# Kernel optimization log

Hardware: AMD Instinct MI355X
Metric: run time of the kernel (lower is better)

## Reference

```python
import jax, jax.numpy as jnp
import numpy as np

B, T, C = 2, 512, 128
H = 4 * C
EPS_LN = 1e-5
EPS_WKV = 1e-6


def setup_inputs() -> dict:
    key = jax.random.key(0)
    ks = jax.random.split(key, 12)
    def rn(i, shape, s):
        return jax.random.normal(ks[i], shape, jnp.float32) * s
    return {
        "x": jax.random.normal(ks[0], (B, T, C), jnp.float32),
        "ln1_g": jnp.ones((C,), jnp.float32), "ln1_b": jnp.zeros((C,), jnp.float32),
        "mu": rn(1, (C,), 0.1),
        "Wr": rn(2, (C, C), 0.02), "br": jnp.zeros((C,), jnp.float32),
        "Wk": rn(3, (C, C), 0.02), "bk": jnp.zeros((C,), jnp.float32),
        "Wv": rn(4, (C, C), 0.02), "bv": jnp.zeros((C,), jnp.float32),
        "w_decay": rn(5, (C,), 0.5),
        "Wo": rn(6, (C, C), 0.02), "bo": jnp.zeros((C,), jnp.float32),
        "ln2_g": jnp.ones((C,), jnp.float32), "ln2_b": jnp.zeros((C,), jnp.float32),
        "W1": rn(7, (C, H), 0.02), "b1": jnp.zeros((H,), jnp.float32),
        "W2": rn(8, (H, C), 0.02), "b2": jnp.zeros((C,), jnp.float32),
    }


def _ln(x, g, b):
    m = x.mean(-1, keepdims=True)
    v = ((x - m) ** 2).mean(-1, keepdims=True)
    return (x - m) * jax.lax.rsqrt(v + EPS_LN) * g + b


def _wkv_dir(k, v, w_lc):
    # k, v: (B,T,C); w_lc: (T,C) per-(position,channel) decay weight
    p = k[:, :, None, :] * w_lc[None, None, :, :]              # (B,T,L,C)
    p = jnp.exp(p - jax.lax.stop_gradient(p.max(-1, keepdims=True)))  # stable, max over C (as in source, dim=-1)
    p = p / (p.sum(-1, keepdims=True) + EPS_WKV)               # normalize over channel dim, as written in torch
    return jnp.einsum('btlc,blc->btc', p, v)


def _forward(x, ln1_g, ln1_b, mu, Wr, br, Wk, bk, Wv, bv, w_decay, Wo, bo, ln2_g, ln2_b, W1, b1, W2, b2):
    Tn = x.shape[1]
    h = _ln(x, ln1_g, ln1_b)
    # TemporalShift: past half shifted right, future half shifted left
    xp, xf = jnp.split(h, 2, axis=-1)
    xp = jnp.pad(xp, ((0, 0), (1, 0), (0, 0)))[:, :-1]
    xf = jnp.pad(xf, ((0, 0), (0, 1), (0, 0)))[:, 1:]
    hs = h + mu * jnp.concatenate([xp, xf], axis=-1)
    r = jax.nn.sigmoid(hs @ Wr + br)
    k = hs @ Wk + bk
    v = hs @ Wv + bv
    t = jnp.arange(Tn, dtype=x.dtype)[:, None]                 # (T,1)
    neg_w = -jnp.exp(w_decay)[None, :]                         # (1,C)
    w_f = neg_w * (Tn - 1 - t) / (Tn - 1)                      # (T,C)
    w_b = neg_w * t / (Tn - 1)                                 # (T,C)
    x_f = _wkv_dir(k, v, w_f)
    x_b = jnp.flip(_wkv_dir(jnp.flip(k, 1), jnp.flip(v, 1), w_b), 1)
    wk = r * (x_f + x_b) * 0.5
    y = x + wk @ Wo + bo
    h2 = _ln(y, ln2_g, ln2_b)
    m = jax.nn.gelu(h2 @ W1 + b1, approximate=False) @ W2 + b2
    return y + m


def reference(x, ln1_g, ln1_b, mu, Wr, br, Wk, bk, Wv, bv, w_decay, Wo, bo, ln2_g, ln2_b, W1, b1, W2, b2):
    return _forward(x, ln1_g, ln1_b, mu, Wr, br, Wk, bk, Wv, bv, w_decay, Wo, bo, ln2_g, ln2_b, W1, b1, W2, b2)
```

## Files before the change

kernel.cpp:

```cpp
#include <hip/hip_runtime.h>
#include <hip/hip_bf16.h>

#define Bq 2
#define Tq 512
#define Cq 128
#define Hq 512
#define NROW (Bq*Tq)

__device__ __forceinline__ float bfbits2f(unsigned short u) {
    return __uint_as_float(((unsigned)u) << 16);
}
__device__ __forceinline__ bool detect_f32(const void* sent) {
    return *(const unsigned*)sent == 0x3F800000u;
}
#define LD(p, i) (f32 ? ((const float*)(p))[i] : bfbits2f(((const unsigned short*)(p))[i]))
__device__ __forceinline__ float4 LD4(const void* p, int i, bool f32) {
    if (f32) return ((const float4*)p)[i >> 2];
    ushort4 u = *(const ushort4*)((const unsigned short*)p + i);
    return make_float4(bfbits2f(u.x), bfbits2f(u.y), bfbits2f(u.z), bfbits2f(u.w));
}

__global__ __launch_bounds__(512) void k2_qkv(
    const void* __restrict__ sent,
    const void* __restrict__ x,
    const void* __restrict__ ln1g, const void* __restrict__ ln1b,
    const void* __restrict__ mu,
    const void* __restrict__ Wr, const void* __restrict__ br,
    const void* __restrict__ Wk, const void* __restrict__ bk,
    const void* __restrict__ Wv, const void* __restrict__ bv,
    const void* __restrict__ wdec,
    float* __restrict__ r_out, float* __restrict__ u_out,
    float* __restrict__ v_out)
{
    const bool f32 = detect_f32(sent);
    int R0 = blockIdx.x * 2, tid = threadIdx.x;
    int g = tid >> 7, col = tid & 127;
    int t0 = R0 & (Tq - 1);
    int bbase = R0 - t0;

    __shared__ float h4[4][Cq];
    __shared__ float hs2[2][Cq];
    __shared__ float part[4][6][Cq];
    __shared__ float wred[8][2];

    {
        int t = t0 - 1 + g;
        int tcl = min(max(t, 0), Tq - 1);
        int row = bbase + tcl;
        float xv = LD(x, row * Cq + col);
        float s1 = xv, s2 = xv * xv;
        for (int off = 32; off; off >>= 1) {
            s1 += __shfl_xor(s1, off);
            s2 += __shfl_xor(s2, off);
        }
        int wid = tid >> 6;
        if ((tid & 63) == 0) { wred[wid][0] = s1; wred[wid][1] = s2; }
        __syncthreads();
        float S1 = wred[2 * g][0] + wred[2 * g + 1][0];
        float S2 = wred[2 * g][1] + wred[2 * g + 1][1];
        float m  = S1 * (1.f / Cq);
        float va = S2 * (1.f / Cq) - m * m;
        float rs = rsqrtf(va + 1e-5f);
        h4[g][col] = (xv - m) * rs * LD(ln1g, col) + LD(ln1b, col);
    }
    __syncthreads();

    if (g < 2) {
        int r2 = g, tt = t0 + r2;
        float hv = h4[r2 + 1][col];
        float nb;
        if (col < Cq / 2) nb = (tt > 0)      ? h4[r2][col]     : 0.f;
        else              nb = (tt < Tq - 1) ? h4[r2 + 2][col] : 0.f;
        hs2[r2][col] = hv + LD(mu, col) * nb;
    }
    __syncthreads();

    {
        float ar0 = 0.f, ar1 = 0.f, ak0 = 0.f, ak1 = 0.f, av0 = 0.f, av1 = 0.f;
        int c0 = g * 32;
        for (int cc = c0; cc < c0 + 32; cc += 4) {
            float4 h0 = *(const float4*)&hs2[0][cc];
            float4 h1 = *(const float4*)&hs2[1][cc];
            float wr0 = LD(Wr, (cc + 0) * Cq + col);
            float wr1 = LD(Wr, (cc + 1) * Cq + col);
            float wr2 = LD(Wr, (cc + 2) * Cq + col);
            float wr3 = LD(Wr, (cc + 3) * Cq + col);
            float wk0 = LD(Wk, (cc + 0) * Cq + col);
            float wk1 = LD(Wk, (cc + 1) * Cq + col);
            float wk2 = LD(Wk, (cc + 2) * Cq + col);
            float wk3 = LD(Wk, (cc + 3) * Cq + col);
            float wv0 = LD(Wv, (cc + 0) * Cq + col);
            float wv1 = LD(Wv, (cc + 1) * Cq + col);
            float wv2 = LD(Wv, (cc + 2) * Cq + col);
            float wv3 = LD(Wv, (cc + 3) * Cq + col);
            ar0 += h0.x * wr0; ar1 += h1.x * wr0;
            ak0 += h0.x * wk0; ak1 += h1.x * wk0;
            av0 += h0.x * wv0; av1 += h1.x * wv0;
            ar0 += h0.y * wr1; ar1 += h1.y * wr1;
            ak0 += h0.y * wk1; ak1 += h1.y * wk1;
            av0 += h0.y * wv1; av1 += h1.y * wv1;
            ar0 += h0.z * wr2; ar1 += h1.z * wr2;
            ak0 += h0.z * wk2; ak1 += h1.z * wk2;
            av0 += h0.z * wv2; av1 += h1.z * wv2;
            ar0 += h0.w * wr3; ar1 += h1.w * wr3;
            ak0 += h0.w * wk3; ak1 += h1.w * wk3;
            av0 += h0.w * wv3; av1 += h1.w * wv3;
        }
        part[g][0][col] = ar0; part[g][1][col] = ar1;
        part[g][2][col] = ak0; part[g][3][col] = ak1;
        part[g][4][col] = av0; part[g][5][col] = av1;
    }
    __syncthreads();

    if (g < 3) {
#pragma unroll
        for (int r2 = 0; r2 < 2; ++r2) {
            int m = 2 * g + r2;
            float a = (part[0][m][col] + part[1][m][col])
                    + (part[2][m][col] + part[3][m][col]);
            int row = R0 + r2;
            if (g == 0) {
                float rr = 1.f / (1.f + __expf(-(a + LD(br, col))));
                r_out[row * Cq + col] = rr;
            } else if (g == 1) {
                float wd = LD(wdec, col);
                wd = fminf(fmaxf(wd, -20.f), 20.f);
                float negw = -__expf(wd);
                float uu = (a + LD(bk, col)) * negw;
                uu = fminf(fmaxf(uu, -30.f), 30.f);
                u_out[row * Cq + col] = uu;
            } else {
                v_out[row * Cq + col] = a + LD(bv, col);
            }
        }
    }
}

__global__ __launch_bounds__(1024) void k34_wkv_ffn(
    const void* __restrict__ sent,
    const float* __restrict__ u_in,
    const float* __restrict__ v_in,
    const float* __restrict__ r_in,
    const void* __restrict__ x,
    const void* __restrict__ Wo, const void* __restrict__ bo,
    const void* __restrict__ lng, const void* __restrict__ lnb,
    const void* __restrict__ W1, const void* __restrict__ b1,
    const void* __restrict__ W2, const void* __restrict__ b2,
    void* __restrict__ out)
{
    const bool f32 = detect_f32(sent);
    int R0 = blockIdx.x * 4, tid = threadIdx.x;
    int b = R0 >> 9;
    const float inv511 = 1.f / (float)(Tq - 1);

    __shared__ float u4[4][Cq];
    __shared__ float rinv[4][Tq];
    __shared__ float vbuf[2][32][Cq];
    __shared__ float pp2[2][4][Cq];
    __shared__ float wk4[4][Cq];
    __shared__ float pwo[2][4][Cq];
    __shared__ float y4[4][Cq];
    __shared__ float h2s[4][Cq];
    __shared__ float part1[4][4][Hq];
    __shared__ float m1s[4][Hq];
    __shared__ float part2[8][4][Cq];
    __shared__ float wred[16][2];

    if (tid < 512) {
        int r = tid >> 7, c = tid & 127;
        u4[r][c] = u_in[(R0 + r) * Cq + c];
    }
    __syncthreads();

    {
        int l = tid & 511, rb = (tid >> 9) * 2;
        float a = (float)(Tq - 1 - l) * inv511 * 1.44269504f;
#pragma unroll
        for (int rr = rb; rr < rb + 2; ++rr) {
            float s0 = 0.f, s1 = 0.f, s2 = 0.f, s3 = 0.f;
            const float4* uu4 = (const float4*)u4[rr];
            for (int cc = 0; cc < Cq / 4; ++cc) {
                float4 uv = uu4[cc];
                s0 += exp2f(a * uv.x);
                s1 += exp2f(a * uv.y);
                s2 += exp2f(a * uv.z);
                s3 += exp2f(a * uv.w);
            }
            rinv[rr][l] = 1.f / ((s0 + s1) + (s2 + s3) + 1e-6f);
        }
    }

    const float4* v4g = (const float4*)v_in + (size_t)b * (Tq * Cq / 4);
    ((float4*)vbuf[0])[tid] = v4g[tid];
    __syncthreads();

    {
        int r = tid >> 8, h = (tid >> 7) & 1, c = tid & 127;
        float uu = u4[r][c];
        float gi1 = __expf(-uu * inv511);
        float gi2 = gi1 * gi1, gi3 = gi2 * gi1, gi4 = gi2 * gi2;
        float gi16 = gi4 * gi4; gi16 *= gi16;
        float gi32 = gi16 * gi16;
        float el0 = __expf(uu * (float)(Tq - 1 - 16 * h) * inv511);
        float a0 = 0.f, a1 = 0.f, a2 = 0.f, a3 = 0.f;
        for (int ci = 0; ci < 16; ++ci) {
            int cur = ci & 1;
            float4 vnext;
            if (ci < 15) vnext = v4g[(ci + 1) * 1024 + tid];
            int lb = ci * 32 + h * 16;
            int lloc = h * 16;
            float el = el0;
#pragma unroll
            for (int q = 0; q < 4; ++q) {
                float4 rv = *(const float4*)&rinv[r][lb + 4 * q];
                float v0 = vbuf[cur][lloc + 4 * q + 0][c];
                float v1 = vbuf[cur][lloc + 4 * q + 1][c];
                float v2 = vbuf[cur][lloc + 4 * q + 2][c];
                float v3 = vbuf[cur][lloc + 4 * q + 3][c];
                a0 += v0 * (el * rv.x);
                a1 += v1 * ((el * gi1) * rv.y);
                a2 += v2 * ((el * gi2) * rv.z);
                a3 += v3 * ((el * gi3) * rv.w);
                el *= gi4;
            }
            el0 *= gi32;
            if (ci < 15) ((float4*)vbuf[cur ^ 1])[tid] = vnext;
            __syncthreads();
        }
        pp2[h][r][c] = (a0 + a1) + (a2 + a3);
    }
    __syncthreads();

    if (tid < 512) {
        int r = tid >> 7, c = tid & 127;
        float acc = pp2[0][r][c] + pp2[1][r][c];
        wk4[r][c] = r_in[(R0 + r) * Cq + c] * acc;
    }
    __syncthreads();

    {
        int r = tid >> 8, ks = (tid >> 7) & 1, c = tid & 127;
        float s = 0.f;
        int k0 = ks * 64;
        for (int kk = k0; kk < k0 + 64; kk += 4) {
            float4 w = *(const float4*)&wk4[r][kk];
            s += w.x * LD(Wo, (kk + 0) * Cq + c);
            s += w.y * LD(Wo, (kk + 1) * Cq + c);
            s += w.z * LD(Wo, (kk + 2) * Cq + c);
            s += w.w * LD(Wo, (kk + 3) * Cq + c);
        }
        pwo[ks][r][c] = s;
    }
    __syncthreads();
    if (tid < 512) {
        int r = tid >> 7, c = tid & 127;
        y4[r][c] = LD(x, (R0 + r) * Cq + c) + pwo[0][r][c] + pwo[1][r][c] + LD(bo, c);
    }
    __syncthreads();

    {
        int r = tid >> 7, c = tid & 127;
        float yv = (tid < 512) ? y4[r][c] : 0.f;
        float s1 = yv, s2 = yv * yv;
        for (int off = 32; off; off >>= 1) {
            s1 += __shfl_xor(s1, off);
            s2 += __shfl_xor(s2, off);
        }
        int wid = tid >> 6;
        if ((tid & 63) == 0) { wred[wid][0] = s1; wred[wid][1] = s2; }
        __syncthreads();
        if (tid < 512) {
            float S1 = wred[2 * r][0] + wred[2 * r + 1][0];
            float S2 = wred[2 * r][1] + wred[2 * r + 1][1];
            float m  = S1 * (1.f / Cq);
            float va = S2 * (1.f / Cq) - m * m;
            float rs = rsqrtf(va + 1e-5f);
            h2s[r][c] = (yv - m) * rs * LD(lng, c) + LD(lnb, c);
        }
    }
    __syncthreads();

    {
        int ks = (tid >> 7) & 3, rh = tid >> 9, j4 = (tid & 127) * 4;
        int ra = 2 * rh, rb2 = 2 * rh + 1;
        float a00 = 0.f, a01 = 0.f, a02 = 0.f, a03 = 0.f;
        float a10 = 0.f, a11 = 0.f, a12 = 0.f, a13 = 0.f;
        int c0 = ks * 32;
        for (int cc = c0; cc < c0 + 32; cc += 4) {
            float4 w0 = LD4(W1, (cc + 0) * Hq + j4, f32);
            float4 w1 = LD4(W1, (cc + 1) * Hq + j4, f32);
            float4 w2 = LD4(W1, (cc + 2) * Hq + j4, f32);
            float4 w3 = LD4(W1, (cc + 3) * Hq + j4, f32);
            float4 ha = *(const float4*)&h2s[ra][cc];
            float4 hb = *(const float4*)&h2s[rb2][cc];
            a00 += ha.x * w0.x; a01 += ha.x * w0.y; a02 += ha.x * w0.z; a03 += ha.x * w0.w;
            a10 += hb.x * w0.x; a11 += hb.x * w0.y; a12 += hb.x * w0.z; a13 += hb.x * w0.w;
            a00 += ha.y * w1.x; a01 += ha.y * w1.y; a02 += ha.y * w1.z; a03 += ha.y * w1.w;
            a10 += hb.y * w1.x; a11 += hb.y * w1.y; a12 += hb.y * w1.z; a13 += hb.y * w1.w;
            a00 += ha.z * w2.x; a01 += ha.z * w2.y; a02 += ha.z * w2.z; a03 += ha.z * w2.w;
            a10 += hb.z * w2.x; a11 += hb.z * w2.y; a12 += hb.z * w2.z; a13 += hb.z * w2.w;
            a00 += ha.w * w3.x; a01 += ha.w * w3.y; a02 += ha.w * w3.z; a03 += ha.w * w3.w;
            a10 += hb.w * w3.x; a11 += hb.w * w3.y; a12 += hb.w * w3.z; a13 += hb.w * w3.w;
        }
        *(float4*)&part1[ks][ra][j4]  = make_float4(a00, a01, a02, a03);
        *(float4*)&part1[ks][rb2][j4] = make_float4(a10, a11, a12, a13);
    }
    __syncthreads();
    {
        int j = tid & 511, rh = tid >> 9;
        float bb = LD(b1, j);
#pragma unroll
        for (int rr = 2 * rh; rr < 2 * rh + 2; ++rr) {
            float xg = ((part1[0][rr][j] + part1[1][rr][j])
                      + (part1[2][rr][j] + part1[3][rr][j])) + bb;
            m1s[rr][j] = 0.5f * xg * (1.f + erff(xg * 0.70710678f));
        }
    }
    __syncthreads();

    {
        int ks = tid >> 7, c = tid & 127;
        int h0 = ks * 64;
        float a0 = 0.f, a1 = 0.f, a2 = 0.f, a3 = 0.f;
        for (int hh = h0; hh < h0 + 64; hh += 4) {
            float4 m0 = *(const float4*)&m1s[0][hh];
            float4 m1v = *(const float4*)&m1s[1][hh];
            float4 m2 = *(const float4*)&m1s[2][hh];
            float4 m3 = *(const float4*)&m1s[3][hh];
            float w0 = LD(W2, (hh + 0) * Cq + c);
            float w1 = LD(W2, (hh + 1) * Cq + c);
            float w2 = LD(W2, (hh + 2) * Cq + c);
            float w3 = LD(W2, (hh + 3) * Cq + c);
            a0 += m0.x * w0; a1 += m1v.x * w0; a2 += m2.x * w0; a3 += m3.x * w0;
            a0 += m0.y * w1; a1 += m1v.y * w1; a2 += m2.y * w1; a3 += m3.y * w1;
            a0 += m0.z * w2; a1 += m1v.z * w2; a2 += m2.z * w2; a3 += m3.z * w2;
            a0 += m0.w * w3; a1 += m1v.w * w3; a2 += m2.w * w3; a3 += m3.w * w3;
        }
        part2[ks][0][c] = a0; part2[ks][1][c] = a1;
        part2[ks][2][c] = a2; part2[ks][3][c] = a3;
    }
    __syncthreads();
    if (tid < 512) {
        int r = tid >> 7, c = tid & 127;
        float s = ((part2[0][r][c] + part2[1][r][c]) + (part2[2][r][c] + part2[3][r][c]))
                + ((part2[4][r][c] + part2[5][r][c]) + (part2[6][r][c] + part2[7][r][c]));
        float val = y4[r][c] + s + LD(b2, c);
        int idx = (R0 + r) * Cq + c;
        if (f32) ((float*)out)[idx] = val;
        else     ((__hip_bfloat16*)out)[idx] = __float2bfloat16(val);
    }
}

extern "C" void kernel_launch(void* const* d_in, const int* in_sizes, int n_in,
                              void* d_out, int out_size, void* d_ws, size_t ws_size,
                              hipStream_t stream)
{
    const void* x    = d_in[0];
    const void* ln1g = d_in[1];
    const void* ln1b = d_in[2];
    const void* mu   = d_in[3];
    const void* Wr   = d_in[4];
    const void* br   = d_in[5];
    const void* Wk   = d_in[6];
    const void* bk   = d_in[7];
    const void* Wv   = d_in[8];
    const void* bv   = d_in[9];
    const void* wdec = d_in[10];
    const void* Wo   = d_in[11];
    const void* bo   = d_in[12];
    const void* ln2g = d_in[13];
    const void* ln2b = d_in[14];
    const void* W1   = d_in[15];
    const void* b1   = d_in[16];
    const void* W2   = d_in[17];
    const void* b2   = d_in[18];

    float* ws = (float*)d_ws;
    float* u  = ws;
    float* r  = ws + 131072;
    float* v  = ws + 262144;

    k2_qkv<<<NROW / 2, 512, 0, stream>>>(ln1g, x, ln1g, ln1b, mu, Wr, br, Wk, bk, Wv, bv, wdec, r, u, v);
    k34_wkv_ffn<<<NROW / 4, 1024, 0, stream>>>(ln1g, u, v, r, x, Wo, bo, ln2g, ln2b, W1, b1, W2, b2, d_out);
}
```

Baseline: 174.2 us.

## Restructure QKV and WKV-FFN kernels with vectorized weight loads and 2-row blocks

The QKV kernel now gives each matrix (Wr, Wk, Wv) its own thread group. Each thread loads float4 weight columns and keeps the two rows interleaved in shared memory, replacing scalar per-column loads. The second kernel moves from 4 rows and 1024 threads to 2 rows and 512 threads per block, doubling the grid to raise occupancy. In that kernel the WKV sum reads v straight from global memory in 8 sequence segments instead of a double-buffered shared tile, and the Wo, W1 and W2 matmuls switch to float4 weight loads with more split-K partials. The cost is that each weight is reused across only two rows instead of four, and the small reductions need extra shared-memory passes.

```diff
diff --git a/kernel.cpp b/kernel.cpp
--- a/kernel.cpp
+++ b/kernel.cpp
@@ -20,7 +20,7 @@
     return make_float4(bfbits2f(u.x), bfbits2f(u.y), bfbits2f(u.z), bfbits2f(u.w));
 }
 
-__global__ __launch_bounds__(512) void k2_qkv(
+__global__ __launch_bounds__(512) void kA_qkv(
     const void* __restrict__ sent,
     const void* __restrict__ x,
     const void* __restrict__ ln1g, const void* __restrict__ ln1b,
@@ -39,8 +39,8 @@
     int bbase = R0 - t0;
 
     __shared__ float h4[4][Cq];
-    __shared__ float hs2[2][Cq];
-    __shared__ float part[4][6][Cq];
+    __shared__ __align__(16) float hsi[Cq][2];
+    __shared__ __align__(16) float part[3][4][Cq][2];
     __shared__ float wred[8][2];
 
     {
@@ -71,53 +71,33 @@
         float nb;
         if (col < Cq / 2) nb = (tt > 0)      ? h4[r2][col]     : 0.f;
         else              nb = (tt < Tq - 1) ? h4[r2 + 2][col] : 0.f;
-        hs2[r2][col] = hv + LD(mu, col) * nb;
-    }
-    __syncthreads();
-
-    {
-        float ar0 = 0.f, ar1 = 0.f, ak0 = 0.f, ak1 = 0.f, av0 = 0.f, av1 = 0.f;
-        int c0 = g * 32;
-        for (int cc = c0; cc < c0 + 32; cc += 4) {
-            float4 h0 = *(const float4*)&hs2[0][cc];
-            float4 h1 = *(const float4*)&hs2[1][cc];
-            float wr0 = LD(Wr, (cc + 0) * Cq + col);
-            float wr1 = LD(Wr, (cc + 1) * Cq + col);
-            float wr2 = LD(Wr, (cc + 2) * Cq + col);
-            float wr3 = LD(Wr, (cc + 3) * Cq + col);
-            float wk0 = LD(Wk, (cc + 0) * Cq + col);
-            float wk1 = LD(Wk, (cc + 1) * Cq + col);
-            float wk2 = LD(Wk, (cc + 2) * Cq + col);
-            float wk3 = LD(Wk, (cc + 3) * Cq + col);
-            float wv0 = LD(Wv, (cc + 0) * Cq + col);
-            float wv1 = LD(Wv, (cc + 1) * Cq + col);
-            float wv2 = LD(Wv, (cc + 2) * Cq + col);
-            float wv3 = LD(Wv, (cc + 3) * Cq + col);
-            ar0 += h0.x * wr0; ar1 += h1.x * wr0;
-            ak0 += h0.x * wk0; ak1 += h1.x * wk0;
-            av0 += h0.x * wv0; av1 += h1.x * wv0;
-            ar0 += h0.y * wr1; ar1 += h1.y * wr1;
-            ak0 += h0.y * wk1; ak1 += h1.y * wk1;
-            av0 += h0.y * wv1; av1 += h1.y * wv1;
-            ar0 += h0.z * wr2; ar1 += h1.z * wr2;
-            ak0 += h0.z * wk2; ak1 += h1.z * wk2;
-            av0 += h0.z * wv2; av1 += h1.z * wv2;
-            ar0 += h0.w * wr3; ar1 += h1.w * wr3;
-            ak0 += h0.w * wk3; ak1 += h1.w * wk3;
-            av0 += h0.w * wv3; av1 += h1.w * wv3;
-        }
-        part[g][0][col] = ar0; part[g][1][col] = ar1;
-        part[g][2][col] = ak0; part[g][3][col] = ak1;
-        part[g][4][col] = av0; part[g][5][col] = av1;
+        hsi[col][r2] = hv + LD(mu, col) * nb;
     }
     __syncthreads();
 
     if (g < 3) {
+        const void* W = (g == 0) ? Wr : (g == 1) ? Wk : Wv;
+        int ks = (tid >> 5) & 3, j0 = (tid & 31) * 4;
+        float a00 = 0.f, a01 = 0.f, a02 = 0.f, a03 = 0.f;
+        float a10 = 0.f, a11 = 0.f, a12 = 0.f, a13 = 0.f;
+        int c0 = ks * 32;
+#pragma unroll 4
+        for (int cc = c0; cc < c0 + 32; ++cc) {
+            float4 w  = LD4(W, cc * Cq + j0, f32);
+            float2 hv = *(const float2*)&hsi[cc][0];
+            a00 += hv.x * w.x; a01 += hv.x * w.y; a02 += hv.x * w.z; a03 += hv.x * w.w;
+            a10 += hv.y * w.x; a11 += hv.y * w.y; a12 += hv.y * w.z; a13 += hv.y * w.w;
+        }
+        *(float4*)&part[g][ks][j0][0]     = make_float4(a00, a10, a01, a11);
+        *(float4*)&part[g][ks][j0 + 2][0] = make_float4(a02, a12, a03, a13);
+    }
+    __syncthreads();
+
+    if (g < 3) {
 #pragma unroll
         for (int r2 = 0; r2 < 2; ++r2) {
-            int m = 2 * g + r2;
-            float a = (part[0][m][col] + part[1][m][col])
-                    + (part[2][m][col] + part[3][m][col]);
+            float a = (part[g][0][col][r2] + part[g][1][col][r2])
+                    + (part[g][2][col][r2] + part[g][3][col][r2]);
             int row = R0 + r2;
             if (g == 0) {
                 float rr = 1.f / (1.f + __expf(-(a + LD(br, col))));
@@ -136,7 +116,7 @@
     }
 }
 
-__global__ __launch_bounds__(1024) void k34_wkv_ffn(
+__global__ __launch_bounds__(512) void kB_wkv_ffn(
     const void* __restrict__ sent,
     const float* __restrict__ u_in,
     const float* __restrict__ v_in,
@@ -149,36 +129,29 @@
     void* __restrict__ out)
 {
     const bool f32 = detect_f32(sent);
-    int R0 = blockIdx.x * 4, tid = threadIdx.x;
+    int R0 = blockIdx.x * 2, tid = threadIdx.x;
     int b = R0 >> 9;
     const float inv511 = 1.f / (float)(Tq - 1);
 
-    __shared__ float u4[4][Cq];
-    __shared__ float rinv[4][Tq];
-    __shared__ float vbuf[2][32][Cq];
-    __shared__ float pp2[2][4][Cq];
-    __shared__ float wk4[4][Cq];
-    __shared__ float pwo[2][4][Cq];
-    __shared__ float y4[4][Cq];
-    __shared__ float h2s[4][Cq];
-    __shared__ float part1[4][4][Hq];
-    __shared__ float m1s[4][Hq];
-    __shared__ float part2[8][4][Cq];
-    __shared__ float wred[16][2];
-
-    if (tid < 512) {
-        int r = tid >> 7, c = tid & 127;
-        u4[r][c] = u_in[(R0 + r) * Cq + c];
-    }
-    __syncthreads();
-
-    {
-        int l = tid & 511, rb = (tid >> 9) * 2;
+    __shared__ float u2[2][Cq];
+    __shared__ __align__(16) float rinv2[Tq][2];
+    __shared__ float part[8][2][Cq];
+    __shared__ __align__(16) float wki[Cq][2];
+    __shared__ __align__(16) float h2i[Cq][2];
+    __shared__ __align__(16) float m1i[Hq][2];
+    __shared__ __align__(16) float pbuf[16 * Cq * 2];
+    __shared__ float wred[8][2];
+
+    if (tid < 256) u2[tid >> 7][tid & 127] = u_in[(R0 + (tid >> 7)) * Cq + (tid & 127)];
+    __syncthreads();
+
+    {
+        int l = tid;
         float a = (float)(Tq - 1 - l) * inv511 * 1.44269504f;
 #pragma unroll
-        for (int rr = rb; rr < rb + 2; ++rr) {
+        for (int r = 0; r < 2; ++r) {
             float s0 = 0.f, s1 = 0.f, s2 = 0.f, s3 = 0.f;
-            const float4* uu4 = (const float4*)u4[rr];
+            const float4* uu4 = (const float4*)u2[r];
             for (int cc = 0; cc < Cq / 4; ++cc) {
                 float4 uv = uu4[cc];
                 s0 += exp2f(a * uv.x);
@@ -186,81 +159,78 @@
                 s2 += exp2f(a * uv.z);
                 s3 += exp2f(a * uv.w);
             }
-            rinv[rr][l] = 1.f / ((s0 + s1) + (s2 + s3) + 1e-6f);
-        }
-    }
-
-    const float4* v4g = (const float4*)v_in + (size_t)b * (Tq * Cq / 4);
-    ((float4*)vbuf[0])[tid] = v4g[tid];
-    __syncthreads();
-
-    {
-        int r = tid >> 8, h = (tid >> 7) & 1, c = tid & 127;
-        float uu = u4[r][c];
-        float gi1 = __expf(-uu * inv511);
-        float gi2 = gi1 * gi1, gi3 = gi2 * gi1, gi4 = gi2 * gi2;
-        float gi16 = gi4 * gi4; gi16 *= gi16;
-        float gi32 = gi16 * gi16;
-        float el0 = __expf(uu * (float)(Tq - 1 - 16 * h) * inv511);
-        float a0 = 0.f, a1 = 0.f, a2 = 0.f, a3 = 0.f;
-        for (int ci = 0; ci < 16; ++ci) {
-            int cur = ci & 1;
-            float4 vnext;
-            if (ci < 15) vnext = v4g[(ci + 1) * 1024 + tid];
-            int lb = ci * 32 + h * 16;
-            int lloc = h * 16;
-            float el = el0;
-#pragma unroll
-            for (int q = 0; q < 4; ++q) {
-                float4 rv = *(const float4*)&rinv[r][lb + 4 * q];
-                float v0 = vbuf[cur][lloc + 4 * q + 0][c];
-                float v1 = vbuf[cur][lloc + 4 * q + 1][c];
-                float v2 = vbuf[cur][lloc + 4 * q + 2][c];
-                float v3 = vbuf[cur][lloc + 4 * q + 3][c];
-                a0 += v0 * (el * rv.x);
-                a1 += v1 * ((el * gi1) * rv.y);
-                a2 += v2 * ((el * gi2) * rv.z);
-                a3 += v3 * ((el * gi3) * rv.w);
-                el *= gi4;
-            }
-            el0 *= gi32;
-            if (ci < 15) ((float4*)vbuf[cur ^ 1])[tid] = vnext;
-            __syncthreads();
-        }
-        pp2[h][r][c] = (a0 + a1) + (a2 + a3);
-    }
-    __syncthreads();
-
-    if (tid < 512) {
+            rinv2[l][r] = 1.f / ((s0 + s1) + (s2 + s3) + 1e-6f);
+        }
+    }
+    __syncthreads();
+
+    {
+        int seg = tid >> 6, cp = tid & 63, c2 = cp * 2;
+        float u00 = u2[0][c2], u01 = u2[0][c2 + 1];
+        float u10 = u2[1][c2], u11 = u2[1][c2 + 1];
+        float jb = (float)(seg * 64);
+        float e00 = __expf(u00 * jb * inv511), e01 = __expf(u01 * jb * inv511);
+        float e10 = __expf(u10 * jb * inv511), e11 = __expf(u11 * jb * inv511);
+        float g00 = __expf(u00 * inv511), g01 = __expf(u01 * inv511);
+        float g10 = __expf(u10 * inv511), g11 = __expf(u11 * inv511);
+        float G00 = g00 * g00, G01 = g01 * g01, G10 = g10 * g10, G11 = g11 * g11;
+        float p00 = 0.f, p01 = 0.f, p10 = 0.f, p11 = 0.f;
+        float q00 = 0.f, q01 = 0.f, q10 = 0.f, q11 = 0.f;
+        const float2* vb = (const float2*)(v_in + (size_t)b * Tq * Cq) + cp;
+        int j0 = seg * 64;
+        for (int j = j0; j < j0 + 64; j += 2) {
+            int l = (Tq - 1) - j;
+            float2 v0 = vb[(size_t)l * 64];
+            float2 v1 = vb[(size_t)(l - 1) * 64];
+            float2 ra = *(const float2*)&rinv2[l][0];
+            float2 rb = *(const float2*)&rinv2[l - 1][0];
+            p00 += v0.x * (e00 * ra.x); p01 += v0.y * (e01 * ra.x);
+            p10 += v0.x * (e10 * ra.y); p11 += v0.y * (e11 * ra.y);
+            q00 += v1.x * ((e00 * g00) * rb.x); q01 += v1.y * ((e01 * g01) * rb.x);
+            q10 += v1.x * ((e10 * g10) * rb.y); q11 += v1.y * ((e11 * g11) * rb.y);
+            e00 *= G00; e01 *= G01; e10 *= G10; e11 *= G11;
+        }
+        part[seg][0][c2]     = p00 + q00;
+        part[seg][0][c2 + 1] = p01 + q01;
+        part[seg][1][c2]     = p10 + q10;
+        part[seg][1][c2 + 1] = p11 + q11;
+    }
+    __syncthreads();
+
+    if (tid < 256) {
         int r = tid >> 7, c = tid & 127;
-        float acc = pp2[0][r][c] + pp2[1][r][c];
-        wk4[r][c] = r_in[(R0 + r) * Cq + c] * acc;
-    }
-    __syncthreads();
-
-    {
-        int r = tid >> 8, ks = (tid >> 7) & 1, c = tid & 127;
+        float acc = ((part[0][r][c] + part[1][r][c]) + (part[2][r][c] + part[3][r][c]))
+                  + ((part[4][r][c] + part[5][r][c]) + (part[6][r][c] + part[7][r][c]));
+        wki[c][r] = r_in[(R0 + r) * Cq + c] * acc;
+    }
+    __syncthreads();
+
+    {
+        int ks = tid >> 5, c0 = (tid & 31) * 4;
+        float a00 = 0.f, a01 = 0.f, a02 = 0.f, a03 = 0.f;
+        float a10 = 0.f, a11 = 0.f, a12 = 0.f, a13 = 0.f;
+        int k0 = ks * 8;
+#pragma unroll
+        for (int cc = k0; cc < k0 + 8; ++cc) {
+            float4 w   = LD4(Wo, cc * Cq + c0, f32);
+            float2 wk2 = *(const float2*)&wki[cc][0];
+            a00 += wk2.x * w.x; a01 += wk2.x * w.y; a02 += wk2.x * w.z; a03 += wk2.x * w.w;
+            a10 += wk2.y * w.x; a11 += wk2.y * w.y; a12 += wk2.y * w.z; a13 += wk2.y * w.w;
+        }
+        *(float4*)&pbuf[(ks * Cq + c0) * 2]     = make_float4(a00, a10, a01, a11);
+        *(float4*)&pbuf[(ks * Cq + c0 + 2) * 2] = make_float4(a02, a12, a03, a13);
+    }
+    __syncthreads();
+
+    float yv = 0.f;
+    if (tid < 256) {
+        int r = tid >> 7, c = tid & 127;
         float s = 0.f;
-        int k0 = ks * 64;
-        for (int kk = k0; kk < k0 + 64; kk += 4) {
-            float4 w = *(const float4*)&wk4[r][kk];
-            s += w.x * LD(Wo, (kk + 0) * Cq + c);
-            s += w.y * LD(Wo, (kk + 1) * Cq + c);
-            s += w.z * LD(Wo, (kk + 2) * Cq + c);
-            s += w.w * LD(Wo, (kk + 3) * Cq + c);
-        }
-        pwo[ks][r][c] = s;
-    }
-    __syncthreads();
-    if (tid < 512) {
-        int r = tid >> 7, c = tid & 127;
-        y4[r][c] = LD(x, (R0 + r) * Cq + c) + pwo[0][r][c] + pwo[1][r][c] + LD(bo, c);
-    }
-    __syncthreads();
-
-    {
-        int r = tid >> 7, c = tid & 127;
-        float yv = (tid < 512) ? y4[r][c] : 0.f;
+#pragma unroll
+        for (int ks = 0; ks < 16; ++ks) s += pbuf[(ks * Cq + c) * 2 + r];
+        yv = LD(x, (R0 + r) * Cq + c) + s + LD(bo, c);
+    }
+    {
         float s1 = yv, s2 = yv * yv;
         for (int off = 32; off; off >>= 1) {
             s1 += __shfl_xor(s1, off);
@@ -269,82 +239,69 @@
         int wid = tid >> 6;
         if ((tid & 63) == 0) { wred[wid][0] = s1; wred[wid][1] = s2; }
         __syncthreads();
-        if (tid < 512) {
+        if (tid < 256) {
+            int r = tid >> 7, c = tid & 127;
             float S1 = wred[2 * r][0] + wred[2 * r + 1][0];
             float S2 = wred[2 * r][1] + wred[2 * r + 1][1];
             float m  = S1 * (1.f / Cq);
             float va = S2 * (1.f / Cq) - m * m;
             float rs = rsqrtf(va + 1e-5f);
-            h2s[r][c] = (yv - m) * rs * LD(lng, c) + LD(lnb, c);
-        }
-    }
-    __syncthreads();
-
-    {
-        int ks = (tid >> 7) & 3, rh = tid >> 9, j4 = (tid & 127) * 4;
-        int ra = 2 * rh, rb2 = 2 * rh + 1;
+            h2i[c][r] = (yv - m) * rs * LD(lng, c) + LD(lnb, c);
+        }
+    }
+    __syncthreads();
+
+    {
+        int ks = tid >> 7, j0 = (tid & 127) * 4;
         float a00 = 0.f, a01 = 0.f, a02 = 0.f, a03 = 0.f;
         float a10 = 0.f, a11 = 0.f, a12 = 0.f, a13 = 0.f;
         int c0 = ks * 32;
-        for (int cc = c0; cc < c0 + 32; cc += 4) {
-            float4 w0 = LD4(W1, (cc + 0) * Hq + j4, f32);
-            float4 w1 = LD4(W1, (cc + 1) * Hq + j4, f32);
-            float4 w2 = LD4(W1, (cc + 2) * Hq + j4, f32);
-            float4 w3 = LD4(W1, (cc + 3) * Hq + j4, f32);
-            float4 ha = *(const float4*)&h2s[ra][cc];
-            float4 hb = *(const float4*)&h2s[rb2][cc];
-            a00 += ha.x * w0.x; a01 += ha.x * w0.y; a02 += ha.x * w0.z; a03 += ha.x * w0.w;
-            a10 += hb.x * w0.x; a11 += hb.x * w0.y; a12 += hb.x * w0.z; a13 += hb.x * w0.w;
-            a00 += ha.y * w1.x; a01 += ha.y * w1.y; a02 += ha.y * w1.z; a03 += ha.y * w1.w;
-            a10 += hb.y * w1.x; a11 += hb.y * w1.y; a12 += hb.y * w1.z; a13 += hb.y * w1.w;
-            a00 += ha.z * w2.x; a01 += ha.z * w2.y; a02 += ha.z * w2.z; a03 += ha.z * w2.w;
-            a10 += hb.z * w2.x; a11 += hb.z * w2.y; a12 += hb.z * w2.z; a13 += hb.z * w2.w;
-            a00 += ha.w * w3.x; a01 += ha.w * w3.y; a02 += ha.w * w3.z; a03 += ha.w * w3.w;
-            a10 += hb.w * w3.x; a11 += hb.w * w3.y; a12 += hb.w * w3.z; a13 += hb.w * w3.w;
-        }
-        *(float4*)&part1[ks][ra][j4]  = make_float4(a00, a01, a02, a03);
-        *(float4*)&part1[ks][rb2][j4] = make_float4(a10, a11, a12, a13);
-    }
-    __syncthreads();
-    {
-        int j = tid & 511, rh = tid >> 9;
+#pragma unroll 4
+        for (int cc = c0; cc < c0 + 32; ++cc) {
+            float4 w  = LD4(W1, cc * Hq + j0, f32);
+            float2 hv = *(const float2*)&h2i[cc][0];
+            a00 += hv.x * w.x; a01 += hv.x * w.y; a02 += hv.x * w.z; a03 += hv.x * w.w;
+            a10 += hv.y * w.x; a11 += hv.y * w.y; a12 += hv.y * w.z; a13 += hv.y * w.w;
+        }
+        *(float4*)&pbuf[(ks * Hq + j0) * 2]     = make_float4(a00, a10, a01, a11);
+        *(float4*)&pbuf[(ks * Hq + j0 + 2) * 2] = make_float4(a02, a12, a03, a13);
+    }
+    __syncthreads();
+    {
+        int j = tid;
         float bb = LD(b1, j);
-#pragma unroll
-        for (int rr = 2 * rh; rr < 2 * rh + 2; ++rr) {
-            float xg = ((part1[0][rr][j] + part1[1][rr][j])
-                      + (part1[2][rr][j] + part1[3][rr][j])) + bb;
-            m1s[rr][j] = 0.5f * xg * (1.f + erff(xg * 0.70710678f));
-        }
-    }
-    __syncthreads();
-
-    {
-        int ks = tid >> 7, c = tid & 127;
-        int h0 = ks * 64;
-        float a0 = 0.f, a1 = 0.f, a2 = 0.f, a3 = 0.f;
-        for (int hh = h0; hh < h0 + 64; hh += 4) {
-            float4 m0 = *(const float4*)&m1s[0][hh];
-            float4 m1v = *(const float4*)&m1s[1][hh];
-            float4 m2 = *(const float4*)&m1s[2][hh];
-            float4 m3 = *(const float4*)&m1s[3][hh];
-            float w0 = LD(W2, (hh + 0) * Cq + c);
-            float w1 = LD(W2, (hh + 1) * Cq + c);
-            float w2 = LD(W2, (hh + 2) * Cq + c);
-            float w3 = LD(W2, (hh + 3) * Cq + c);
-            a0 += m0.x * w0; a1 += m1v.x * w0; a2 += m2.x * w0; a3 += m3.x * w0;
-            a0 += m0.y * w1; a1 += m1v.y * w1; a2 += m2.y * w1; a3 += m3.y * w1;
-            a0 += m0.z * w2; a1 += m1v.z * w2; a2 += m2.z * w2; a3 += m3.z * w2;
-            a0 += m0.w * w3; a1 += m1v.w * w3; a2 += m2.w * w3; a3 += m3.w * w3;
-        }
-        part2[ks][0][c] = a0; part2[ks][1][c] = a1;
-        part2[ks][2][c] = a2; part2[ks][3][c] = a3;
-    }
-    __syncthreads();
-    if (tid < 512) {
+        float x0 = ((pbuf[(0 * Hq + j) * 2]     + pbuf[(1 * Hq + j) * 2])
+                  + (pbuf[(2 * Hq + j) * 2]     + pbuf[(3 * Hq + j) * 2])) + bb;
+        float x1 = ((pbuf[(0 * Hq + j) * 2 + 1] + pbuf[(1 * Hq + j) * 2 + 1])
+                  + (pbuf[(2 * Hq + j) * 2 + 1] + pbuf[(3 * Hq + j) * 2 + 1])) + bb;
+        m1i[j][0] = 0.5f * x0 * (1.f + erff(x0 * 0.70710678f));
+        m1i[j][1] = 0.5f * x1 * (1.f + erff(x1 * 0.70710678f));
+    }
+    __syncthreads();
+
+    {
+        int ks = tid >> 5, c0 = (tid & 31) * 4;
+        float a00 = 0.f, a01 = 0.f, a02 = 0.f, a03 = 0.f;
+        float a10 = 0.f, a11 = 0.f, a12 = 0.f, a13 = 0.f;
+        int h0 = ks * 32;
+#pragma unroll 4
+        for (int hh = h0; hh < h0 + 32; ++hh) {
+            float4 w  = LD4(W2, hh * Cq + c0, f32);
+            float2 mv = *(const float2*)&m1i[hh][0];
+            a00 += mv.x * w.x; a01 += mv.x * w.y; a02 += mv.x * w.z; a03 += mv.x * w.w;
+            a10 += mv.y * w.x; a11 += mv.y * w.y; a12 += mv.y * w.z; a13 += mv.y * w.w;
+        }
+        __syncthreads();
+        *(float4*)&pbuf[(ks * Cq + c0) * 2]     = make_float4(a00, a10, a01, a11);
+        *(float4*)&pbuf[(ks * Cq + c0 + 2) * 2] = make_float4(a02, a12, a03, a13);
+    }
+    __syncthreads();
+    if (tid < 256) {
         int r = tid >> 7, c = tid & 127;
-        float s = ((part2[0][r][c] + part2[1][r][c]) + (part2[2][r][c] + part2[3][r][c]))
-                + ((part2[4][r][c] + part2[5][r][c]) + (part2[6][r][c] + part2[7][r][c]));
-        float val = y4[r][c] + s + LD(b2, c);
+        float s = 0.f;
+#pragma unroll
+        for (int ks = 0; ks < 16; ++ks) s += pbuf[(ks * Cq + c) * 2 + r];
+        float val = yv + s + LD(b2, c);
         int idx = (R0 + r) * Cq + c;
         if (f32) ((float*)out)[idx] = val;
         else     ((__hip_bfloat16*)out)[idx] = __float2bfloat16(val);
@@ -380,6 +337,6 @@
     float* r  = ws + 131072;
     float* v  = ws + 262144;
 
-    k2_qkv<<<NROW / 2, 512, 0, stream>>>(ln1g, x, ln1g, ln1b, mu, Wr, br, Wk, bk, Wv, bv, wdec, r, u, v);
-    k34_wkv_ffn<<<NROW / 4, 1024, 0, stream>>>(ln1g, u, v, r, x, Wo, bo, ln2g, ln2b, W1, b1, W2, b2, d_out);
-}
+    kA_qkv<<<NROW / 2, 512, 0, stream>>>(ln1g, x, ln1g, ln1b, mu, Wr, br, Wk, bk, Wv, bv, wdec, r, u, v);
+    kB_wkv_ffn<<<NROW / 2, 512, 0, stream>>>(ln1g, u, v, r, x, Wo, bo, ln2g, ln2b, W1, b1, W2, b2, d_out);
+}
```

After: 156.3 us. 10.3% less time.
